# Kernel optimization log

Measured on AMD Instinct MI355X. Metric: run time of the kernel, lower is better.

The kernel has to match this reference:

```python
import jax, jax.numpy as jnp
import numpy as np

EMBED_DIM = 1024
HEAD_NUM = 16
HEAD_DIM = EMBED_DIM // HEAD_NUM
T, B, S = 2048, 4, 2048


def setup_inputs() -> dict:
    key = jax.random.key(0)
    ks = jax.random.split(key, 11)
    s = 0.02
    return {
        "query": jax.random.normal(ks[0], (T, B, EMBED_DIM), jnp.float32),
        "key": jax.random.normal(ks[1], (S, B, EMBED_DIM), jnp.float32),
        "value": jax.random.normal(ks[2], (S, B, EMBED_DIM), jnp.float32),
        "q_proj_weight": jax.random.normal(ks[3], (EMBED_DIM, EMBED_DIM), jnp.float32) * s,
        "k_proj_weight": jax.random.normal(ks[4], (EMBED_DIM, EMBED_DIM), jnp.float32) * s,
        "v_proj_weight": jax.random.normal(ks[5], (EMBED_DIM, EMBED_DIM), jnp.float32) * s,
        "in_proj_bias": jax.random.normal(ks[6], (3 * EMBED_DIM,), jnp.float32) * s,
        "bias_k": jax.random.normal(ks[7], (1, 1, EMBED_DIM), jnp.float32) * s,
        "bias_v": jax.random.normal(ks[8], (1, 1, EMBED_DIM), jnp.float32) * s,
        "out_proj_weight": jax.random.normal(ks[9], (EMBED_DIM, EMBED_DIM), jnp.float32) * s,
        "out_proj_bias": jax.random.normal(ks[10], (EMBED_DIM,), jnp.float32) * s,
    }


def reference(query, key, value, q_proj_weight, k_proj_weight, v_proj_weight,
              in_proj_bias, bias_k, bias_v, out_proj_weight, out_proj_bias):
    t, b, e = query.shape
    h, hd = HEAD_NUM, HEAD_DIM
    scaling = float(hd) ** -0.5
    # input projections (F.linear: x @ W.T + b)
    q = (query @ q_proj_weight.T + in_proj_bias[:e]) * scaling          # [T,B,E]
    k = key @ k_proj_weight.T + in_proj_bias[e:2 * e]                   # [S,B,E]
    v = value @ v_proj_weight.T + in_proj_bias[2 * e:]                  # [S,B,E]
    # append bias_k / bias_v token along the sequence dim
    k = jnp.concatenate([k, jnp.broadcast_to(bias_k, (1, b, e))], axis=0)  # [S+1,B,E]
    v = jnp.concatenate([v, jnp.broadcast_to(bias_v, (1, b, e))], axis=0)  # [S+1,B,E]
    # split heads: [L, B, E] -> [B*H, L, hd]
    q = q.reshape(t, b * h, hd).transpose(1, 0, 2)
    k = k.reshape(-1, b * h, hd).transpose(1, 0, 2)
    v = v.reshape(-1, b * h, hd).transpose(1, 0, 2)
    # full O(T*S) attention, as in the original bmm->softmax->bmm
    weights = jax.nn.softmax(jnp.einsum('nqd,nkd->nqk', q, k), axis=-1)  # [B*H,T,S+1]
    out = jnp.einsum('nqk,nkd->nqd', weights, v)                         # [B*H,T,hd]
    out = out.transpose(1, 0, 2).reshape(t, b, e)
    out = out @ out_proj_weight.T + out_proj_bias
    avg_weights = weights.sum(axis=1) / h                                # [B*H,S+1]
    return out, avg_weights
```

## Files before the change

### kernel.cpp

```cpp
#include <hip/hip_runtime.h>

#define T_DIM 2048
#define B_DIM 4
#define S_DIM 2048
#define E_DIM 1024
#define H_NUM 16
#define HD    64
#define NH    64
#define SP1   2049
#define SPAD  2112
#define NCHUNK 33

typedef short bf16x8 __attribute__((ext_vector_type(8)));
typedef float f32x4  __attribute__((ext_vector_type(4)));
typedef float f32x16 __attribute__((ext_vector_type(16)));
typedef unsigned int u32;

#define QSCALE 0.18033688011112042f

#if __has_builtin(__builtin_amdgcn_exp2f)
__device__ __forceinline__ float exp2_fast(float x) { return __builtin_amdgcn_exp2f(x); }
#else
__device__ __forceinline__ float exp2_fast(float x) { return __expf(x * 0.6931471805599453f); }
#endif

__device__ __forceinline__ unsigned short f2bf(float x) {
    union { float f; unsigned int u; } v; v.f = x;
    unsigned int r = v.u + 0x7FFFu + ((v.u >> 16) & 1u);
    return (unsigned short)(r >> 16);
}

__device__ __forceinline__ u32 cvtpk_bf16(float lo, float hi) {
    u32 r;
    asm("v_cvt_pk_bf16_f32 %0, %1, %2" : "=v"(r) : "v"(lo), "v"(hi));
    return r;
}
__device__ __forceinline__ void plswap(u32& a, u32& b) {
    asm("v_permlane32_swap_b32 %0, %1" : "+v"(a), "+v"(b));
}

__global__ __launch_bounds__(256)
void cvt_bf16_k(const float* __restrict__ src, short* __restrict__ dst, int n8)
{
    int i = blockIdx.x * 256 + threadIdx.x;
    if (i >= n8) return;
    const float4* s = reinterpret_cast<const float4*>(src) + (size_t)i * 2;
    float4 a = s[0], b = s[1];
    bf16x8 o;
    o[0] = (short)f2bf(a.x); o[1] = (short)f2bf(a.y);
    o[2] = (short)f2bf(a.z); o[3] = (short)f2bf(a.w);
    o[4] = (short)f2bf(b.x); o[5] = (short)f2bf(b.y);
    o[6] = (short)f2bf(b.z); o[7] = (short)f2bf(b.w);
    *(reinterpret_cast<bf16x8*>(dst) + i) = o;
}

template<int MODE>
__global__ __launch_bounds__(256)
void gemm_bf16(const void* __restrict__ Ap, const short* __restrict__ W,
               const float* __restrict__ bias, void* __restrict__ outp)
{
    __shared__ short As[128][72];
    __shared__ short Bs[128][72];
    const int bm = blockIdx.x, bn = blockIdx.y;
    const int tid = threadIdx.x;
    const int l = tid & 63, w = tid >> 6;
    const int wr = w >> 1, wc = w & 1;
    const int lr = l & 15, lg = l >> 4;
    const int rb = tid >> 3, cg = tid & 7;

    float4 paA[4], paB[4];
    bf16x8 pa3[4];
    bf16x8 pb[4];

    auto load_tiles = [&](int k0) {
#pragma unroll
        for (int it = 0; it < 4; ++it) {
            const int row = it * 32 + rb;
            if (MODE == 3) {
                const int m = bm * 128 + row;
                const size_t asrc =
                    ((size_t)((m & 3) * 16 + (k0 >> 6)) * T_DIM + (m >> 2)) * HD + cg * 8;
                pa3[it] = *reinterpret_cast<const bf16x8*>((const short*)Ap + asrc);
            } else {
                const float* ap = (const float*)Ap + (size_t)(bm * 128 + row) * E_DIM + k0 + cg * 8;
                paA[it] = *reinterpret_cast<const float4*>(ap);
                paB[it] = *reinterpret_cast<const float4*>(ap + 4);
            }
            pb[it] = *reinterpret_cast<const bf16x8*>(
                W + (size_t)(bn * 128 + row) * E_DIM + k0 + cg * 8);
        }
    };
    auto write_tiles = [&]() {
#pragma unroll
        for (int it = 0; it < 4; ++it) {
            const int row = it * 32 + rb;
            if (MODE == 3) {
                *reinterpret_cast<bf16x8*>(&As[row][cg * 8]) = pa3[it];
            } else {
                uint4 st;
                st.x = cvtpk_bf16(paA[it].x, paA[it].y); st.y = cvtpk_bf16(paA[it].z, paA[it].w);
                st.z = cvtpk_bf16(paB[it].x, paB[it].y); st.w = cvtpk_bf16(paB[it].z, paB[it].w);
                *reinterpret_cast<uint4*>(&As[row][cg * 8]) = st;
            }
            *reinterpret_cast<bf16x8*>(&Bs[row][cg * 8]) = pb[it];
        }
    };

    load_tiles(0);
    write_tiles();
    __syncthreads();

    f32x4 acc[4][4] = {};

    for (int k0 = 0; k0 < E_DIM; k0 += 64) {
        const bool more = (k0 + 64 < E_DIM);
        if (more) load_tiles(k0 + 64);

        __builtin_amdgcn_s_setprio(1);
#pragma unroll
        for (int c = 0; c < 2; ++c) {
            bf16x8 af[4], bf[4];
#pragma unroll
            for (int mi = 0; mi < 4; ++mi)
                af[mi] = *reinterpret_cast<const bf16x8*>(&As[wr * 64 + mi * 16 + lr][c * 32 + lg * 8]);
#pragma unroll
            for (int ni = 0; ni < 4; ++ni)
                bf[ni] = *reinterpret_cast<const bf16x8*>(&Bs[wc * 64 + ni * 16 + lr][c * 32 + lg * 8]);
#pragma unroll
            for (int mi = 0; mi < 4; ++mi)
#pragma unroll
                for (int ni = 0; ni < 4; ++ni)
                    acc[mi][ni] = __builtin_amdgcn_mfma_f32_16x16x32_bf16(
                        af[mi], bf[ni], acc[mi][ni], 0, 0, 0);
        }
        __builtin_amdgcn_s_setprio(0);

        if (more) {
            __syncthreads();
            write_tiles();
            __syncthreads();
        }
    }

#pragma unroll
    for (int mi = 0; mi < 4; ++mi)
#pragma unroll
        for (int ni = 0; ni < 4; ++ni) {
            const int colg = bn * 128 + wc * 64 + ni * 16 + lr;
            const float bv = bias[colg];
#pragma unroll
            for (int r = 0; r < 4; ++r) {
                const int m = bm * 128 + wr * 64 + mi * 16 + lg * 4 + r;
                float v = acc[mi][ni][r] + bv;
                if (MODE == 3) {
                    ((float*)outp)[(size_t)m * E_DIM + colg] = v;
                } else {
                    if (MODE == 0) v *= QSCALE;
                    const int seq = m >> 2, b = m & 3;
                    const int head = colg >> 6, d = colg & 63;
                    const int sd = (MODE == 0) ? T_DIM : SPAD;
                    ((short*)outp)[((size_t)(b * 16 + head) * sd + seq) * HD + d] = (short)f2bf(v);
                }
            }
        }
}

__global__ void fill_kv_pad(short* __restrict__ k_h, short* __restrict__ v_h,
                            const float* __restrict__ bias_k,
                            const float* __restrict__ bias_v)
{
    const int d   = threadIdx.x;
    const int row = S_DIM + blockIdx.x;
    const int n   = blockIdx.y;
    short bk = 0, bv = 0;
    if (row == S_DIM) {
        bk = (short)f2bf(bias_k[(n & 15) * HD + d]);
        bv = (short)f2bf(bias_v[(n & 15) * HD + d]);
    }
    const size_t idx = ((size_t)n * SPAD + row) * HD + d;
    k_h[idx] = bk;
    v_h[idx] = bv;
}

__global__ __launch_bounds__(256)
void attn_mfma(const short* __restrict__ q_h, const short* __restrict__ k_h,
               const short* __restrict__ v_h, short* __restrict__ o_h,
               float* __restrict__ m_arr, float* __restrict__ l_arr)
{
    __shared__ short KsD[2][64 * 64];
    __shared__ short VtD[2][64 * 64];

    const int id = blockIdx.x;
    const int xcd = id & 7, slot = id >> 3;
    const int n = xcd * 8 + (slot >> 4);
    const int q0 = (slot & 15) * 128;

    const int tid = threadIdx.x, l = tid & 63, w = tid >> 6;
    const int ql = l & 31;
    const int hi = l >> 5;
    const int qrow = q0 + w * 32 + ql;

    const int krow = tid >> 3, kcg = tid & 7;
    const int kswz = (kcg * 16) ^ ((krow & 7) << 4);
    const int sp = tid & 31, d0 = (tid >> 5) * 8;

    const short* kbase = k_h + (size_t)n * SPAD * HD;
    const short* vbase = v_h + (size_t)n * SPAD * HD;

    bf16x8 aq0, aq1, aq2, aq3;
    {
        const short* qp = q_h + ((size_t)n * T_DIM + qrow) * HD + hi * 8;
        aq0 = *(const bf16x8*)(qp);
        aq1 = *(const bf16x8*)(qp + 16);
        aq2 = *(const bf16x8*)(qp + 32);
        aq3 = *(const bf16x8*)(qp + 48);
    }

    bf16x8 pk0 = *(const bf16x8*)(kbase + (size_t)krow * HD + kcg * 8);
    bf16x8 pk1 = *(const bf16x8*)(kbase + (size_t)(32 + krow) * HD + kcg * 8);
    bf16x8 pv0 = *(const bf16x8*)(vbase + (size_t)(2 * sp) * HD + d0);
    bf16x8 pv1 = *(const bf16x8*)(vbase + (size_t)(2 * sp + 1) * HD + d0);
    {
        char* KsB = (char*)KsD[0];
        char* VtB = (char*)VtD[0];
        *(bf16x8*)(KsB + krow * 128 + kswz) = pk0;
        *(bf16x8*)(KsB + (32 + krow) * 128 + kswz) = pk1;
#pragma unroll
        for (int j = 0; j < 8; ++j) {
            u32 pk = (u32)(unsigned short)pv0[j] | ((u32)(unsigned short)pv1[j] << 16);
            const int d = d0 + j;
            *(u32*)(VtB + d * 128 + ((4 * sp) ^ ((d & 7) << 4))) = pk;
        }
    }
    __syncthreads();

    float m_run = -1e30f, l_run = 0.f;
    f32x16 accA, accB;
#pragma unroll
    for (int r = 0; r < 16; ++r) { accA[r] = 0.f; accB[r] = 0.f; }

    for (int kc = 0; kc < NCHUNK; ++kc) {
        const char* KsB = (const char*)KsD[kc & 1];
        const char* VtB = (const char*)VtD[kc & 1];
        const bool more = (kc + 1 < NCHUNK);

        if (more) {
            const int s0n = (kc + 1) * 64;
            pk0 = *(const bf16x8*)(kbase + (size_t)(s0n + krow) * HD + kcg * 8);
            pk1 = *(const bf16x8*)(kbase + (size_t)(s0n + 32 + krow) * HD + kcg * 8);
            pv0 = *(const bf16x8*)(vbase + (size_t)(s0n + 2 * sp) * HD + d0);
            pv1 = *(const bf16x8*)(vbase + (size_t)(s0n + 2 * sp + 1) * HD + d0);
        }

        f32x16 sc0, sc1;
#pragma unroll
        for (int r = 0; r < 16; ++r) { sc0[r] = 0.f; sc1[r] = 0.f; }
        __builtin_amdgcn_s_setprio(1);
#pragma unroll
        for (int sl = 0; sl < 4; ++sl) {
            const int cb = ((sl * 32) + hi * 16) ^ ((ql & 7) << 4);
            bf16x8 kf0 = *(const bf16x8*)(KsB + ql * 128 + cb);
            bf16x8 kf1 = *(const bf16x8*)(KsB + (32 + ql) * 128 + cb);
            bf16x8 qf = (sl == 0) ? aq0 : (sl == 1) ? aq1 : (sl == 2) ? aq2 : aq3;
            sc0 = __builtin_amdgcn_mfma_f32_32x32x16_bf16(kf0, qf, sc0, 0, 0, 0);
            sc1 = __builtin_amdgcn_mfma_f32_32x32x16_bf16(kf1, qf, sc1, 0, 0, 0);
        }
        __builtin_amdgcn_s_setprio(0);

        const int s0 = kc * 64;
        if (s0 + 64 > SP1) {
#pragma unroll
            for (int r = 0; r < 16; ++r) {
                const int key = (r & 3) + 8 * (r >> 2) + 4 * hi;
                if (s0 + key >= SP1)      sc0[r] = -1e30f;
                if (s0 + 32 + key >= SP1) sc1[r] = -1e30f;
            }
        }

        float mx = sc0[0];
#pragma unroll
        for (int r = 1; r < 16; ++r) mx = fmaxf(mx, sc0[r]);
#pragma unroll
        for (int r = 0; r < 16; ++r) mx = fmaxf(mx, sc1[r]);
        mx = fmaxf(mx, __shfl_xor(mx, 32));
        if (!__all(mx - m_run <= 8.0f)) {
            const float mnew = fmaxf(m_run, mx);
            const float fac = exp2_fast(m_run - mnew);
            l_run *= fac;
#pragma unroll
            for (int r = 0; r < 16; ++r) { accA[r] *= fac; accB[r] *= fac; }
            m_run = mnew;
        }
        float ps = 0.f;
        float p0[16], p1[16];
#pragma unroll
        for (int r = 0; r < 16; ++r) { p0[r] = exp2_fast(sc0[r] - m_run); ps += p0[r]; }
#pragma unroll
        for (int r = 0; r < 16; ++r) { p1[r] = exp2_fast(sc1[r] - m_run); ps += p1[r]; }
        ps += __shfl_xor(ps, 32);
        l_run += ps;

        union PF { u32 u[4]; bf16x8 v; };
        PF pf0, pf1, pf2, pf3;
        {
            u32 a0 = cvtpk_bf16(p0[0], p0[1]),   b0 = cvtpk_bf16(p0[4], p0[5]);   plswap(a0, b0);
            u32 a1 = cvtpk_bf16(p0[2], p0[3]),   b1 = cvtpk_bf16(p0[6], p0[7]);   plswap(a1, b1);
            u32 a2 = cvtpk_bf16(p0[8], p0[9]),   b2 = cvtpk_bf16(p0[12], p0[13]); plswap(a2, b2);
            u32 a3 = cvtpk_bf16(p0[10], p0[11]), b3 = cvtpk_bf16(p0[14], p0[15]); plswap(a3, b3);
            pf0.u[0] = a0; pf0.u[1] = a1; pf0.u[2] = b0; pf0.u[3] = b1;
            pf1.u[0] = a2; pf1.u[1] = a3; pf1.u[2] = b2; pf1.u[3] = b3;
            u32 c0 = cvtpk_bf16(p1[0], p1[1]),   d0_ = cvtpk_bf16(p1[4], p1[5]);   plswap(c0, d0_);
            u32 c1 = cvtpk_bf16(p1[2], p1[3]),   d1_ = cvtpk_bf16(p1[6], p1[7]);   plswap(c1, d1_);
            u32 c2 = cvtpk_bf16(p1[8], p1[9]),   d2_ = cvtpk_bf16(p1[12], p1[13]); plswap(c2, d2_);
            u32 c3 = cvtpk_bf16(p1[10], p1[11]), d3_ = cvtpk_bf16(p1[14], p1[15]); plswap(c3, d3_);
            pf2.u[0] = c0; pf2.u[1] = c1; pf2.u[2] = d0_; pf2.u[3] = d1_;
            pf3.u[0] = c2; pf3.u[1] = c3; pf3.u[2] = d2_; pf3.u[3] = d3_;
        }

        __builtin_amdgcn_s_setprio(1);
#pragma unroll
        for (int ksl = 0; ksl < 4; ++ksl) {
            const int cb = ((ksl * 32) + hi * 16) ^ ((ql & 7) << 4);
            bf16x8 vf0 = *(const bf16x8*)(VtB + ql * 128 + cb);
            bf16x8 vf1 = *(const bf16x8*)(VtB + (32 + ql) * 128 + cb);
            const bf16x8 pv = (ksl == 0) ? pf0.v : (ksl == 1) ? pf1.v : (ksl == 2) ? pf2.v : pf3.v;
            accA = __builtin_amdgcn_mfma_f32_32x32x16_bf16(vf0, pv, accA, 0, 0, 0);
            accB = __builtin_amdgcn_mfma_f32_32x32x16_bf16(vf1, pv, accB, 0, 0, 0);
        }
        __builtin_amdgcn_s_setprio(0);

        if (more) {
            char* KsN = (char*)KsD[(kc & 1) ^ 1];
            char* VtN = (char*)VtD[(kc & 1) ^ 1];
            *(bf16x8*)(KsN + krow * 128 + kswz) = pk0;
            *(bf16x8*)(KsN + (32 + krow) * 128 + kswz) = pk1;
#pragma unroll
            for (int j = 0; j < 8; ++j) {
                u32 pk = (u32)(unsigned short)pv0[j] | ((u32)(unsigned short)pv1[j] << 16);
                const int d = d0 + j;
                *(u32*)(VtN + d * 128 + ((4 * sp) ^ ((d & 7) << 4))) = pk;
            }
            __syncthreads();
        }
    }

    const float il = 1.0f / l_run;
    short* orow = o_h + ((size_t)n * T_DIM + qrow) * HD;
#pragma unroll
    for (int rq = 0; rq < 4; ++rq) {
        uint2 st;
        st.x = cvtpk_bf16(accA[rq * 4 + 0] * il, accA[rq * 4 + 1] * il);
        st.y = cvtpk_bf16(accA[rq * 4 + 2] * il, accA[rq * 4 + 3] * il);
        *(uint2*)(orow + rq * 8 + hi * 4) = st;
        uint2 st2;
        st2.x = cvtpk_bf16(accB[rq * 4 + 0] * il, accB[rq * 4 + 1] * il);
        st2.y = cvtpk_bf16(accB[rq * 4 + 2] * il, accB[rq * 4 + 3] * il);
        *(uint2*)(orow + 32 + rq * 8 + hi * 4) = st2;
    }
    if (hi == 0) {
        m_arr[n * T_DIM + qrow] = m_run;
        l_arr[n * T_DIM + qrow] = l_run;
    }
}

__global__ __launch_bounds__(256)
void colsum_mfma(const short* __restrict__ q_h, const short* __restrict__ k_h,
                 const float* __restrict__ m_arr, const float* __restrict__ l_arr,
                 float* __restrict__ avg_out)
{
    __shared__ short Qs[2][64][72];
    __shared__ float msh[2][64];
    __shared__ float lih[2][64];

    const int id = blockIdx.x;
    const int xcd = id & 7, slot = id >> 3;
    const int n = xcd * 8 + slot / 33;
    const int s0 = (slot % 33) * 64;

    const int tid = threadIdx.x, l = tid & 63, w = tid >> 6;
    const int lr = l & 15, lg = l >> 4;
    const int qr = tid >> 3, qcg = tid & 7;

    const short* qbase = q_h + (size_t)n * T_DIM * HD;

    bf16x8 ak[2];
#pragma unroll
    for (int c = 0; c < 2; ++c)
        ak[c] = *reinterpret_cast<const bf16x8*>(
            k_h + ((size_t)n * SPAD + s0 + w * 16 + lr) * HD + c * 32 + lg * 8);

    bf16x8 qa = *(const bf16x8*)(qbase + (size_t)qr * HD + qcg * 8);
    bf16x8 qb = *(const bf16x8*)(qbase + (size_t)(32 + qr) * HD + qcg * 8);
    float mlv = 0.f;
    if (tid < 64) mlv = m_arr[n * T_DIM + tid];
    else if (tid < 128) mlv = l_arr[n * T_DIM + tid - 64];
    *(bf16x8*)&Qs[0][qr][qcg * 8] = qa;
    *(bf16x8*)&Qs[0][32 + qr][qcg * 8] = qb;
    if (tid < 64) msh[0][tid] = mlv;
    else if (tid < 128) lih[0][tid - 64] = 1.0f / mlv;
    __syncthreads();

    float csum[4] = {0.f, 0.f, 0.f, 0.f};

    for (int it = 0; it < T_DIM / 64; ++it) {
        const int buf = it & 1;
        const bool more = (it + 1 < T_DIM / 64);
        if (more) {
            const int qo = (it + 1) * 64;
            qa = *(const bf16x8*)(qbase + (size_t)(qo + qr) * HD + qcg * 8);
            qb = *(const bf16x8*)(qbase + (size_t)(qo + 32 + qr) * HD + qcg * 8);
            if (tid < 64) mlv = m_arr[n * T_DIM + qo + tid];
            else if (tid < 128) mlv = l_arr[n * T_DIM + qo + tid - 64];
        }
        __builtin_amdgcn_s_setprio(1);
#pragma unroll
        for (int qt = 0; qt < 4; ++qt) {
            bf16x8 bq0 = *reinterpret_cast<const bf16x8*>(&Qs[buf][qt * 16 + lr][lg * 8]);
            bf16x8 bq1 = *reinterpret_cast<const bf16x8*>(&Qs[buf][qt * 16 + lr][32 + lg * 8]);
            f32x4 z = {0.f, 0.f, 0.f, 0.f};
            z = __builtin_amdgcn_mfma_f32_16x16x32_bf16(ak[0], bq0, z, 0, 0, 0);
            z = __builtin_amdgcn_mfma_f32_16x16x32_bf16(ak[1], bq1, z, 0, 0, 0);
            const float mq = msh[buf][qt * 16 + lr];
            const float lq = lih[buf][qt * 16 + lr];
#pragma unroll
            for (int r = 0; r < 4; ++r)
                csum[r] += exp2_fast(z[r] - mq) * lq;
        }
        __builtin_amdgcn_s_setprio(0);
        if (more) {
            *(bf16x8*)&Qs[buf ^ 1][qr][qcg * 8] = qa;
            *(bf16x8*)&Qs[buf ^ 1][32 + qr][qcg * 8] = qb;
            if (tid < 64) msh[buf ^ 1][tid] = mlv;
            else if (tid < 128) lih[buf ^ 1][tid - 64] = 1.0f / mlv;
            __syncthreads();
        }
    }

#pragma unroll
    for (int r = 0; r < 4; ++r) {
        float v = csum[r];
        v += __shfl_xor(v, 1, 16);
        v += __shfl_xor(v, 2, 16);
        v += __shfl_xor(v, 4, 16);
        v += __shfl_xor(v, 8, 16);
        if (lr == 0) {
            const int key = s0 + w * 16 + lg * 4 + r;
            if (key < SP1) avg_out[(size_t)n * SP1 + key] = v * 0.0625f;
        }
    }
}

extern "C" void kernel_launch(void* const* d_in, const int* in_sizes, int n_in,
                              void* d_out, int out_size, void* d_ws, size_t ws_size,
                              hipStream_t stream)
{
    const float* query   = (const float*)d_in[0];
    const float* key     = (const float*)d_in[1];
    const float* value   = (const float*)d_in[2];
    const float* wq      = (const float*)d_in[3];
    const float* wk      = (const float*)d_in[4];
    const float* wv      = (const float*)d_in[5];
    const float* in_bias = (const float*)d_in[6];
    const float* bias_k  = (const float*)d_in[7];
    const float* bias_v  = (const float*)d_in[8];
    const float* wo      = (const float*)d_in[9];
    const float* out_b   = (const float*)d_in[10];
    float* out = (float*)d_out;

    short* wqb = (short*)d_ws;
    short* wkb = wqb + (size_t)E_DIM * E_DIM;
    short* wvb = wkb + (size_t)E_DIM * E_DIM;
    short* wob = wvb + (size_t)E_DIM * E_DIM;
    short* q_h = wob + (size_t)E_DIM * E_DIM;
    short* k_h = q_h + (size_t)NH * T_DIM * HD;
    short* v_h = k_h + (size_t)NH * SPAD * HD;
    short* o_h = v_h + (size_t)NH * SPAD * HD;
    float* m_arr = (float*)(o_h + (size_t)NH * T_DIM * HD);
    float* l_arr = m_arr + (size_t)NH * T_DIM;

    const int n8_w = E_DIM * E_DIM / 8;
    const dim3 blk(256);
    hipLaunchKernelGGL(cvt_bf16_k, dim3((n8_w + 255) / 256), blk, 0, stream, wq, wqb, n8_w);
    hipLaunchKernelGGL(cvt_bf16_k, dim3((n8_w + 255) / 256), blk, 0, stream, wk, wkb, n8_w);
    hipLaunchKernelGGL(cvt_bf16_k, dim3((n8_w + 255) / 256), blk, 0, stream, wv, wvb, n8_w);
    hipLaunchKernelGGL(cvt_bf16_k, dim3((n8_w + 255) / 256), blk, 0, stream, wo, wob, n8_w);

    const dim3 gg(64, 8);
    hipLaunchKernelGGL((gemm_bf16<0>), gg, blk, 0, stream, (const void*)query, wqb, in_bias,             (void*)q_h);
    hipLaunchKernelGGL((gemm_bf16<1>), gg, blk, 0, stream, (const void*)key,   wkb, in_bias + E_DIM,     (void*)k_h);
    hipLaunchKernelGGL((gemm_bf16<2>), gg, blk, 0, stream, (const void*)value, wvb, in_bias + 2 * E_DIM, (void*)v_h);
    hipLaunchKernelGGL(fill_kv_pad, dim3(SPAD - S_DIM, NH), dim3(64), 0, stream,
                       k_h, v_h, bias_k, bias_v);
    hipLaunchKernelGGL(attn_mfma, dim3(1024), blk, 0, stream,
                       q_h, k_h, v_h, o_h, m_arr, l_arr);
    hipLaunchKernelGGL(colsum_mfma, dim3(2112), blk, 0, stream,
                       q_h, k_h, m_arr, l_arr, out + (size_t)T_DIM * B_DIM * E_DIM);
    hipLaunchKernelGGL((gemm_bf16<3>), gg, blk, 0, stream, (const void*)o_h, wob, out_b, (void*)out);
}
```

Before: 309.6 us.

## Batch weight conversion and QKV GEMMs, widen attention blocks to 512 threads

Merges the four weight-conversion launches into one 2D-grid kernel that uses packed bf16 conversion instructions, and merges the three QKV projection GEMMs into a single launch with a z-dimension that selects the input, weight and output. The attention kernel now runs 512-thread blocks, each covering 256 query rows, so every K/V chunk staged in shared memory is reused by twice as many rows. Each thread now loads half as much K/V per chunk. The row max and row sum reductions become tree reductions to shorten the dependency chain. The aim is lower launch overhead and more K/V reuse, at the cost of higher register pressure under launch_bounds(512,4) and fewer attention blocks in the grid.

Result: faster. 294.1 us (-5.0%).

```diff
diff --git a/kernel.cpp b/kernel.cpp
--- a/kernel.cpp
+++ b/kernel.cpp
@@ -12,6 +12,7 @@
 #define NCHUNK 33
 
 typedef short bf16x8 __attribute__((ext_vector_type(8)));
+typedef short bf16x4 __attribute__((ext_vector_type(4)));
 typedef float f32x4  __attribute__((ext_vector_type(4)));
 typedef float f32x16 __attribute__((ext_vector_type(16)));
 typedef unsigned int u32;
@@ -40,28 +41,36 @@
 }
 
 __global__ __launch_bounds__(256)
-void cvt_bf16_k(const float* __restrict__ src, short* __restrict__ dst, int n8)
+void cvt_w4(const float* __restrict__ w0, const float* __restrict__ w1,
+            const float* __restrict__ w2, const float* __restrict__ w3,
+            short* __restrict__ dst)
 {
-    int i = blockIdx.x * 256 + threadIdx.x;
-    if (i >= n8) return;
+    const int y = blockIdx.y;
+    const float* src = (y == 0) ? w0 : (y == 1) ? w1 : (y == 2) ? w2 : w3;
+    short* d = dst + (size_t)y * E_DIM * E_DIM;
+    const int i = blockIdx.x * 256 + threadIdx.x;
     const float4* s = reinterpret_cast<const float4*>(src) + (size_t)i * 2;
     float4 a = s[0], b = s[1];
-    bf16x8 o;
-    o[0] = (short)f2bf(a.x); o[1] = (short)f2bf(a.y);
-    o[2] = (short)f2bf(a.z); o[3] = (short)f2bf(a.w);
-    o[4] = (short)f2bf(b.x); o[5] = (short)f2bf(b.y);
-    o[6] = (short)f2bf(b.z); o[7] = (short)f2bf(b.w);
-    *(reinterpret_cast<bf16x8*>(dst) + i) = o;
+    uint4 o;
+    o.x = cvtpk_bf16(a.x, a.y); o.y = cvtpk_bf16(a.z, a.w);
+    o.z = cvtpk_bf16(b.x, b.y); o.w = cvtpk_bf16(b.z, b.w);
+    *(reinterpret_cast<uint4*>(d) + i) = o;
 }
 
 template<int MODE>
 __global__ __launch_bounds__(256)
-void gemm_bf16(const void* __restrict__ Ap, const short* __restrict__ W,
-               const float* __restrict__ bias, void* __restrict__ outp)
+void gemm_bf16(const void* __restrict__ Xq, const void* __restrict__ Xk,
+               const void* __restrict__ Xv, const short* __restrict__ Wall,
+               const float* __restrict__ biasAll, void* __restrict__ outp)
 {
     __shared__ short As[128][72];
     __shared__ short Bs[128][72];
     const int bm = blockIdx.x, bn = blockIdx.y;
+    const int z = (MODE == 0) ? blockIdx.z : 0;
+    const void* Ap = (MODE == 3) ? Xq : (z == 0) ? Xq : (z == 1) ? Xk : Xv;
+    const short* W = Wall + (size_t)z * E_DIM * E_DIM;
+    const float* bias = biasAll + z * E_DIM;
+
     const int tid = threadIdx.x;
     const int l = tid & 63, w = tid >> 6;
     const int wr = w >> 1, wc = w & 1;
@@ -155,11 +164,14 @@
                 if (MODE == 3) {
                     ((float*)outp)[(size_t)m * E_DIM + colg] = v;
                 } else {
-                    if (MODE == 0) v *= QSCALE;
+                    if (z == 0) v *= QSCALE;
                     const int seq = m >> 2, b = m & 3;
                     const int head = colg >> 6, d = colg & 63;
-                    const int sd = (MODE == 0) ? T_DIM : SPAD;
-                    ((short*)outp)[((size_t)(b * 16 + head) * sd + seq) * HD + d] = (short)f2bf(v);
+                    const int sd = (z == 0) ? T_DIM : SPAD;
+                    short* ob = (short*)outp;
+                    if (z == 1) ob += (size_t)NH * T_DIM * HD;
+                    else if (z == 2) ob += (size_t)NH * T_DIM * HD + (size_t)NH * SPAD * HD;
+                    ob[((size_t)(b * 16 + head) * sd + seq) * HD + d] = (short)f2bf(v);
                 }
             }
         }
@@ -182,7 +194,7 @@
     v_h[idx] = bv;
 }
 
-__global__ __launch_bounds__(256)
+__global__ __launch_bounds__(512, 4)
 void attn_mfma(const short* __restrict__ q_h, const short* __restrict__ k_h,
                const short* __restrict__ v_h, short* __restrict__ o_h,
                float* __restrict__ m_arr, float* __restrict__ l_arr)
@@ -192,8 +204,8 @@
 
     const int id = blockIdx.x;
     const int xcd = id & 7, slot = id >> 3;
-    const int n = xcd * 8 + (slot >> 4);
-    const int q0 = (slot & 15) * 128;
+    const int n = xcd * 8 + (slot >> 3);
+    const int q0 = (slot & 7) * 256;
 
     const int tid = threadIdx.x, l = tid & 63, w = tid >> 6;
     const int ql = l & 31;
@@ -202,7 +214,7 @@
 
     const int krow = tid >> 3, kcg = tid & 7;
     const int kswz = (kcg * 16) ^ ((krow & 7) << 4);
-    const int sp = tid & 31, d0 = (tid >> 5) * 8;
+    const int sp = tid & 31, dq = tid >> 5;
 
     const short* kbase = k_h + (size_t)n * SPAD * HD;
     const short* vbase = v_h + (size_t)n * SPAD * HD;
@@ -216,20 +228,18 @@
         aq3 = *(const bf16x8*)(qp + 48);
     }
 
-    bf16x8 pk0 = *(const bf16x8*)(kbase + (size_t)krow * HD + kcg * 8);
-    bf16x8 pk1 = *(const bf16x8*)(kbase + (size_t)(32 + krow) * HD + kcg * 8);
-    bf16x8 pv0 = *(const bf16x8*)(vbase + (size_t)(2 * sp) * HD + d0);
-    bf16x8 pv1 = *(const bf16x8*)(vbase + (size_t)(2 * sp + 1) * HD + d0);
+    bf16x8 pk  = *(const bf16x8*)(kbase + (size_t)krow * HD + kcg * 8);
+    bf16x4 pva = *(const bf16x4*)(vbase + (size_t)(2 * sp) * HD + dq * 4);
+    bf16x4 pvb = *(const bf16x4*)(vbase + (size_t)(2 * sp + 1) * HD + dq * 4);
     {
         char* KsB = (char*)KsD[0];
         char* VtB = (char*)VtD[0];
-        *(bf16x8*)(KsB + krow * 128 + kswz) = pk0;
-        *(bf16x8*)(KsB + (32 + krow) * 128 + kswz) = pk1;
-#pragma unroll
-        for (int j = 0; j < 8; ++j) {
-            u32 pk = (u32)(unsigned short)pv0[j] | ((u32)(unsigned short)pv1[j] << 16);
-            const int d = d0 + j;
-            *(u32*)(VtB + d * 128 + ((4 * sp) ^ ((d & 7) << 4))) = pk;
+        *(bf16x8*)(KsB + krow * 128 + kswz) = pk;
+#pragma unroll
+        for (int j = 0; j < 4; ++j) {
+            u32 pkd = (u32)(unsigned short)pva[j] | ((u32)(unsigned short)pvb[j] << 16);
+            const int d = dq * 4 + j;
+            *(u32*)(VtB + d * 128 + ((4 * sp) ^ ((d & 7) << 4))) = pkd;
         }
     }
     __syncthreads();
@@ -246,10 +256,9 @@
 
         if (more) {
             const int s0n = (kc + 1) * 64;
-            pk0 = *(const bf16x8*)(kbase + (size_t)(s0n + krow) * HD + kcg * 8);
-            pk1 = *(const bf16x8*)(kbase + (size_t)(s0n + 32 + krow) * HD + kcg * 8);
-            pv0 = *(const bf16x8*)(vbase + (size_t)(s0n + 2 * sp) * HD + d0);
-            pv1 = *(const bf16x8*)(vbase + (size_t)(s0n + 2 * sp + 1) * HD + d0);
+            pk  = *(const bf16x8*)(kbase + (size_t)(s0n + krow) * HD + kcg * 8);
+            pva = *(const bf16x4*)(vbase + (size_t)(s0n + 2 * sp) * HD + dq * 4);
+            pvb = *(const bf16x4*)(vbase + (size_t)(s0n + 2 * sp + 1) * HD + dq * 4);
         }
 
         f32x16 sc0, sc1;
@@ -277,12 +286,14 @@
             }
         }
 
-        float mx = sc0[0];
-#pragma unroll
-        for (int r = 1; r < 16; ++r) mx = fmaxf(mx, sc0[r]);
-#pragma unroll
-        for (int r = 0; r < 16; ++r) mx = fmaxf(mx, sc1[r]);
-        mx = fmaxf(mx, __shfl_xor(mx, 32));
+        float mv[16];
+#pragma unroll
+        for (int r = 0; r < 16; ++r) mv[r] = fmaxf(sc0[r], sc1[r]);
+#pragma unroll
+        for (int s = 8; s > 0; s >>= 1)
+#pragma unroll
+            for (int r = 0; r < s; ++r) mv[r] = fmaxf(mv[r], mv[r + s]);
+        float mx = fmaxf(mv[0], __shfl_xor(mv[0], 32));
         if (!__all(mx - m_run <= 8.0f)) {
             const float mnew = fmaxf(m_run, mx);
             const float fac = exp2_fast(m_run - mnew);
@@ -291,14 +302,19 @@
             for (int r = 0; r < 16; ++r) { accA[r] *= fac; accB[r] *= fac; }
             m_run = mnew;
         }
-        float ps = 0.f;
         float p0[16], p1[16];
 #pragma unroll
-        for (int r = 0; r < 16; ++r) { p0[r] = exp2_fast(sc0[r] - m_run); ps += p0[r]; }
-#pragma unroll
-        for (int r = 0; r < 16; ++r) { p1[r] = exp2_fast(sc1[r] - m_run); ps += p1[r]; }
-        ps += __shfl_xor(ps, 32);
-        l_run += ps;
+        for (int r = 0; r < 16; ++r) p0[r] = exp2_fast(sc0[r] - m_run);
+#pragma unroll
+        for (int r = 0; r < 16; ++r) p1[r] = exp2_fast(sc1[r] - m_run);
+        float sv[16];
+#pragma unroll
+        for (int r = 0; r < 16; ++r) sv[r] = p0[r] + p1[r];
+#pragma unroll
+        for (int s = 8; s > 0; s >>= 1)
+#pragma unroll
+            for (int r = 0; r < s; ++r) sv[r] += sv[r + s];
+        l_run += sv[0] + __shfl_xor(sv[0], 32);
 
         union PF { u32 u[4]; bf16x8 v; };
         PF pf0, pf1, pf2, pf3;
@@ -332,13 +348,12 @@
         if (more) {
             char* KsN = (char*)KsD[(kc & 1) ^ 1];
             char* VtN = (char*)VtD[(kc & 1) ^ 1];
-            *(bf16x8*)(KsN + krow * 128 + kswz) = pk0;
-            *(bf16x8*)(KsN + (32 + krow) * 128 + kswz) = pk1;
-#pragma unroll
-            for (int j = 0; j < 8; ++j) {
-                u32 pk = (u32)(unsigned short)pv0[j] | ((u32)(unsigned short)pv1[j] << 16);
-                const int d = d0 + j;
-                *(u32*)(VtN + d * 128 + ((4 * sp) ^ ((d & 7) << 4))) = pk;
+            *(bf16x8*)(KsN + krow * 128 + kswz) = pk;
+#pragma unroll
+            for (int j = 0; j < 4; ++j) {
+                u32 pkd = (u32)(unsigned short)pva[j] | ((u32)(unsigned short)pvb[j] << 16);
+                const int d = dq * 4 + j;
+                *(u32*)(VtN + d * 128 + ((4 * sp) ^ ((d & 7) << 4))) = pkd;
             }
             __syncthreads();
         }
@@ -468,32 +483,27 @@
     float* out = (float*)d_out;
 
     short* wqb = (short*)d_ws;
-    short* wkb = wqb + (size_t)E_DIM * E_DIM;
-    short* wvb = wkb + (size_t)E_DIM * E_DIM;
-    short* wob = wvb + (size_t)E_DIM * E_DIM;
-    short* q_h = wob + (size_t)E_DIM * E_DIM;
+    short* wob = wqb + (size_t)3 * E_DIM * E_DIM;
+    short* q_h = wqb + (size_t)4 * E_DIM * E_DIM;
     short* k_h = q_h + (size_t)NH * T_DIM * HD;
     short* v_h = k_h + (size_t)NH * SPAD * HD;
     short* o_h = v_h + (size_t)NH * SPAD * HD;
     float* m_arr = (float*)(o_h + (size_t)NH * T_DIM * HD);
     float* l_arr = m_arr + (size_t)NH * T_DIM;
 
-    const int n8_w = E_DIM * E_DIM / 8;
     const dim3 blk(256);
-    hipLaunchKernelGGL(cvt_bf16_k, dim3((n8_w + 255) / 256), blk, 0, stream, wq, wqb, n8_w);
-    hipLaunchKernelGGL(cvt_bf16_k, dim3((n8_w + 255) / 256), blk, 0, stream, wk, wkb, n8_w);
-    hipLaunchKernelGGL(cvt_bf16_k, dim3((n8_w + 255) / 256), blk, 0, stream, wv, wvb, n8_w);
-    hipLaunchKernelGGL(cvt_bf16_k, dim3((n8_w + 255) / 256), blk, 0, stream, wo, wob, n8_w);
-
-    const dim3 gg(64, 8);
-    hipLaunchKernelGGL((gemm_bf16<0>), gg, blk, 0, stream, (const void*)query, wqb, in_bias,             (void*)q_h);
-    hipLaunchKernelGGL((gemm_bf16<1>), gg, blk, 0, stream, (const void*)key,   wkb, in_bias + E_DIM,     (void*)k_h);
-    hipLaunchKernelGGL((gemm_bf16<2>), gg, blk, 0, stream, (const void*)value, wvb, in_bias + 2 * E_DIM, (void*)v_h);
+    hipLaunchKernelGGL(cvt_w4, dim3(512, 4), blk, 0, stream, wq, wk, wv, wo, wqb);
+
+    hipLaunchKernelGGL((gemm_bf16<0>), dim3(64, 8, 3), blk, 0, stream,
+                       (const void*)query, (const void*)key, (const void*)value,
+                       wqb, in_bias, (void*)q_h);
     hipLaunchKernelGGL(fill_kv_pad, dim3(SPAD - S_DIM, NH), dim3(64), 0, stream,
                        k_h, v_h, bias_k, bias_v);
-    hipLaunchKernelGGL(attn_mfma, dim3(1024), blk, 0, stream,
+    hipLaunchKernelGGL(attn_mfma, dim3(512), dim3(512), 0, stream,
                        q_h, k_h, v_h, o_h, m_arr, l_arr);
     hipLaunchKernelGGL(colsum_mfma, dim3(2112), blk, 0, stream,
                        q_h, k_h, m_arr, l_arr, out + (size_t)T_DIM * B_DIM * E_DIM);
-    hipLaunchKernelGGL((gemm_bf16<3>), gg, blk, 0, stream, (const void*)o_h, wob, out_b, (void*)out);
-}
+    hipLaunchKernelGGL((gemm_bf16<3>), dim3(64, 8), blk, 0, stream,
+                       (const void*)o_h, (const void*)o_h, (const void*)o_h,
+                       wob, out_b, (void*)out);
+}
```
